# Optimization experiments

Measured on AMD Instinct MI355X. Metric: run time of the kernel, lower is better.

## Reference

```python
import jax, jax.numpy as jnp
import numpy as np

DIM = 1024
CTX_DIM = 768

def setup_inputs() -> dict:
    key = jax.random.key(0)
    ks = jax.random.split(key, 12)
    B, Sq, Skv = 8, 2048, 2048
    s_d = 1.0 / np.sqrt(DIM)
    s_c = 1.0 / np.sqrt(CTX_DIM)
    return {
        "x": jax.random.normal(ks[0], (B, Sq, DIM), jnp.float32),
        "context": jax.random.normal(ks[1], (B, Skv, CTX_DIM), jnp.float32),
        # nn.Linear weights are [out_features, in_features]
        "Wq": jax.random.uniform(ks[2], (DIM, DIM), jnp.float32, -s_d, s_d),
        "bq": jax.random.uniform(ks[3], (DIM,), jnp.float32, -s_d, s_d),
        "Wk": jax.random.uniform(ks[4], (DIM, CTX_DIM), jnp.float32, -s_c, s_c),
        "bk": jax.random.uniform(ks[5], (DIM,), jnp.float32, -s_c, s_c),
        "Wv": jax.random.uniform(ks[6], (DIM, CTX_DIM), jnp.float32, -s_c, s_c),
        "bv": jax.random.uniform(ks[7], (DIM,), jnp.float32, -s_c, s_c),
        "Wo": jax.random.uniform(ks[8], (DIM, DIM), jnp.float32, -s_d, s_d),
        "bo": jax.random.uniform(ks[9], (DIM,), jnp.float32, -s_d, s_d),
    }

def reference(x, context, Wq, bq, Wk, bk, Wv, bv, Wo, bo):
    # q: [B,Sq,D], k,v: [B,Skv,D]
    q = jnp.einsum('bsi,di->bsd', x, Wq) + bq
    k = jnp.einsum('bsc,dc->bsd', context, Wk) + bk
    v = jnp.einsum('bsc,dc->bsd', context, Wv) + bv
    scale = 1.0 / jnp.sqrt(jnp.asarray(q.shape[-1], q.dtype))
    scores = jnp.einsum('bqd,bkd->bqk', q, k) * scale  # [B,Sq,Skv]
    att = jax.nn.softmax(scores, axis=-1)
    out = jnp.einsum('bqk,bkd->bqd', att, v)
    return jnp.einsum('bqd,od->bqo', out, Wo) + bo
```

## Files before the change

### kernel.cpp

```cpp
#include <hip/hip_runtime.h>

typedef unsigned short u16;
typedef unsigned int   u32;
typedef __attribute__((ext_vector_type(8))) short short8;
typedef __attribute__((ext_vector_type(4))) float f32x4;

#define DIM   1024
#define CDIM  768
#define BATCH 8
#define SQ    2048
#define SKV   2048

__device__ __forceinline__ u16 f2bf(float f) {
    union { float f; u32 u; } c; c.f = f;
    u32 u = c.u;
    u += 0x7fffu + ((u >> 16) & 1u);
    return (u16)(u >> 16);
}

__device__ __forceinline__ void async_copy16(const u16* g, u16* l) {
    __builtin_amdgcn_global_load_lds(
        (const __attribute__((address_space(1))) void*)g,
        (__attribute__((address_space(3))) void*)l,
        16, 0, 0);
}

__device__ __forceinline__ void cvt4(const float* s, u16* d, int i) {
    float4 f = ((const float4*)s)[i];
    ushort4 o;
    o.x = f2bf(f.x); o.y = f2bf(f.y); o.z = f2bf(f.z); o.w = f2bf(f.w);
    ((ushort4*)d)[i] = o;
}

__global__ __launch_bounds__(256)
void conv_xc(const float* __restrict__ x, const float* __restrict__ ctx,
             u16* __restrict__ dx, u16* __restrict__ dc)
{
    int i = blockIdx.x * 256 + threadIdx.x;
    if (i < 4194304) cvt4(x, dx, i);
    else             cvt4(ctx, dc, i - 4194304);
}

__global__ __launch_bounds__(256)
void conv_w(const float* __restrict__ Wq, const float* __restrict__ Wk,
            const float* __restrict__ Wv, const float* __restrict__ Wo,
            u16* __restrict__ dq, u16* __restrict__ dk,
            u16* __restrict__ dv, u16* __restrict__ dw)
{
    int i = blockIdx.x * 256 + threadIdx.x;
    if      (i < 262144) cvt4(Wq, dq, i);
    else if (i < 458752) cvt4(Wk, dk, i - 262144);
    else if (i < 655360) cvt4(Wv, dv, i - 458752);
    else                 cvt4(Wo, dw, i - 655360);
}

__device__ __forceinline__ void stage_half(const u16* __restrict__ G, long ld, long k0,
                                           u16* lbase, int h, int w, int lane)
{
    const int srow = lane >> 3;
    const int sch  = (lane & 7) ^ srow;
#pragma unroll
    for (int q = 0; q < 2; ++q) {
        int rb = h * 128 + q * 64 + w * 8;
        async_copy16(G + (long)(rb + srow) * ld + k0 + sch * 8, lbase + rb * 64);
    }
}


#define BARRIER()                                                              \
    do {                                                                       \
        asm volatile("" ::: "memory");                                         \
        __builtin_amdgcn_s_barrier();                                          \
        asm volatile("" ::: "memory");                                         \
    } while (0)

#define LOAD_A(Xs, mh)                                                         \
    do {                                                                       \
        _Pragma("unroll") for (int kc = 0; kc < 2; ++kc)                       \
        _Pragma("unroll") for (int i = 0; i < 4; ++i) {                        \
            int R = wm * 128 + (mh) * 64 + i * 16 + l15;                       \
            a[kc][i] = *(const short8*)&(Xs)[R * 64 +                          \
                         (((kc * 4 + quad) ^ (l15 & 7)) * 8)];                 \
        }                                                                      \
    } while (0)

#define LOAD_B(Xs, nh, dst)                                                    \
    do {                                                                       \
        _Pragma("unroll") for (int kc = 0; kc < 2; ++kc)                       \
        _Pragma("unroll") for (int j = 0; j < 2; ++j) {                        \
            int R = wn * 64 + (nh) * 32 + j * 16 + l15;                        \
            dst[kc][j] = *(const short8*)&(Xs)[R * 64 +                        \
                         (((kc * 4 + quad) ^ (l15 & 7)) * 8)];                 \
        }                                                                      \
    } while (0)

#define MFMA_Q(mh, nh, bb)                                                     \
    do {                                                                       \
        _Pragma("unroll") for (int kc = 0; kc < 2; ++kc)                       \
        _Pragma("unroll") for (int i = 0; i < 4; ++i)                          \
        _Pragma("unroll") for (int j = 0; j < 2; ++j)                          \
            acc[(mh) * 4 + i][(nh) * 2 + j] =                                  \
                __builtin_amdgcn_mfma_f32_16x16x32_bf16(                       \
                    a[kc][i], bb[kc][j],                                       \
                    acc[(mh) * 4 + i][(nh) * 2 + j], 0, 0, 0);                 \
    } while (0)

#define TILE_ITER(CUR, TT)                                                     \
    do {                                                                       \
        u16* As = &smem[CUR][0][0];                                            \
        u16* Bs = &smem[CUR][1][0];                                            \
        u16* An = &smem[(CUR) ^ 1][0][0];                                      \
                                                \
        LOAD_A(As, 0);                                                         \
        LOAD_B(Bs, 0, b0);                                                     \
        if ((TT) + 1 < NT)                                                     \
            stage_half(gA, lda, ((long)(TT) + 1) * 64, An, 0, w, lane);        \
        BARRIER();                                                             \
        asm volatile("s_waitcnt lgkmcnt(0)" ::: "memory");                     \
        __builtin_amdgcn_s_setprio(1);                                         \
        MFMA_Q(0, 0, b0);                                                      \
        __builtin_amdgcn_s_setprio(0);                                         \
        BARRIER();                                                             \
                                                \
        LOAD_B(Bs, 1, b1);                                                     \
        if ((TT) + 1 < NT)                                                     \
            stage_half(gA, lda, ((long)(TT) + 1) * 64, An, 1, w, lane);        \
        BARRIER();                                                             \
        asm volatile("s_waitcnt lgkmcnt(0)" ::: "memory");                     \
        __builtin_amdgcn_s_setprio(1);                                         \
        MFMA_Q(0, 1, b1);                                                      \
        __builtin_amdgcn_s_setprio(0);                                         \
        BARRIER();                                                             \
                                                \
        LOAD_A(As, 1);                                                         \
        if ((TT) + 2 < NT)                                                     \
            stage_half(gB, ldb, ((long)(TT) + 2) * 64, Bs, 0, w, lane);        \
        BARRIER();                                                             \
        asm volatile("s_waitcnt lgkmcnt(0)" ::: "memory");                     \
        __builtin_amdgcn_s_setprio(1);                                         \
        MFMA_Q(1, 0, b0);                                                      \
        __builtin_amdgcn_s_setprio(0);                                         \
        BARRIER();                                                             \
                                                \
        if ((TT) + 2 < NT) {                                                   \
            stage_half(gB, ldb, ((long)(TT) + 2) * 64, Bs, 1, w, lane);        \
            asm volatile("s_waitcnt vmcnt(4)" ::: "memory");                   \
        } else if ((TT) + 1 < NT) {                                            \
            asm volatile("s_waitcnt vmcnt(0)" ::: "memory");                   \
        }                                                                      \
        __builtin_amdgcn_sched_barrier(0);                                     \
        BARRIER();                                                             \
        __builtin_amdgcn_s_setprio(1);                                         \
        MFMA_Q(1, 1, b1);                                                      \
        __builtin_amdgcn_s_setprio(0);                                         \
        BARRIER();                                                             \
    } while (0)

template<int BIAS_MODE, int OUT_MODE>
__global__ __launch_bounds__(512, 2)
void gemm_nt(const u16* __restrict__ A, int lda_, long sA,
             const u16* __restrict__ Bw, int ldb_, long sB,
             const float* __restrict__ bias,
             void* __restrict__ Cout, int ldc_, long sC,
             int K, float scale, float* __restrict__ lsum)
{
    __shared__ u16 smem[2][2][256 * 64];
    const int t    = threadIdx.x;
    const int lane = t & 63;
    const int w    = t >> 6;
    const int wm   = w >> 2;
    const int wn   = w & 3;
    const int l15  = lane & 15;
    const int quad = lane >> 4;
    const long lda = lda_, ldb = ldb_, ldc = ldc_;
    const long m0 = (long)blockIdx.x * 256;
    const long n0 = (long)blockIdx.y * 256;
    const u16* gA = A  + (long)blockIdx.z * sA + m0 * lda;
    const u16* gB = Bw + (long)blockIdx.z * sB + n0 * ldb;
    const int NT = K >> 6;

    short8 a[2][4], b0[2][2], b1[2][2];
    const f32x4 fz = {0.f, 0.f, 0.f, 0.f};
    f32x4 acc[8][4];
#pragma unroll
    for (int i = 0; i < 8; ++i)
#pragma unroll
        for (int j = 0; j < 4; ++j) acc[i][j] = fz;

    stage_half(gA, lda, 0, &smem[0][0][0], 0, w, lane);
    stage_half(gA, lda, 0, &smem[0][0][0], 1, w, lane);
    stage_half(gB, ldb, 0, &smem[0][1][0], 0, w, lane);
    stage_half(gB, ldb, 0, &smem[0][1][0], 1, w, lane);
    if (NT > 1) {
        stage_half(gB, ldb, 64, &smem[1][1][0], 0, w, lane);
        stage_half(gB, ldb, 64, &smem[1][1][0], 1, w, lane);
        asm volatile("s_waitcnt vmcnt(4)" ::: "memory");
    } else {
        asm volatile("s_waitcnt vmcnt(0)" ::: "memory");
    }
    __builtin_amdgcn_sched_barrier(0);
    BARRIER();

    for (int T = 0; T < NT; T += 2) {
        TILE_ITER(0, T);
        TILE_ITER(1, T + 1);
    }

    float invl[8][4];
    if (BIAS_MODE == 3) {
        const long lbase = (long)blockIdx.z * (long)gridDim.x * 256 + m0 + wm * 128;
#pragma unroll
        for (int mi = 0; mi < 8; ++mi)
#pragma unroll
            for (int r = 0; r < 4; ++r)
                invl[mi][r] = 1.f / lsum[lbase + mi * 16 + quad * 4 + r];
    }

    float rowpart[8][4];
    if (OUT_MODE == 2) {
#pragma unroll
        for (int mi = 0; mi < 8; ++mi)
#pragma unroll
            for (int r = 0; r < 4; ++r) rowpart[mi][r] = 0.f;
    }

#pragma unroll
    for (int mi = 0; mi < 8; ++mi) {
#pragma unroll
        for (int nj = 0; nj < 4; ++nj) {
            long n = n0 + wn * 64 + nj * 16 + l15;
#pragma unroll
            for (int r = 0; r < 4; ++r) {
                long m = m0 + wm * 128 + mi * 16 + quad * 4 + r;
                float v = acc[mi][nj][r];
                if (BIAS_MODE == 0) v += bias[n];
                else if (BIAS_MODE == 1) v += bias[m];
                v *= scale;
                if (OUT_MODE == 2) { v = __expf(v); rowpart[mi][r] += v; }
                if (BIAS_MODE == 3) v *= invl[mi][r];
                long off = (long)blockIdx.z * sC + m * ldc + n;
                if (OUT_MODE == 1) ((float*)Cout)[off] = v;
                else               ((u16*)Cout)[off]   = f2bf(v);
            }
        }
    }

    if (OUT_MODE == 2) {
#pragma unroll
        for (int mi = 0; mi < 8; ++mi)
#pragma unroll
            for (int r = 0; r < 4; ++r) {
                float p = rowpart[mi][r];
                p += __shfl_xor(p, 1);
                p += __shfl_xor(p, 2);
                p += __shfl_xor(p, 4);
                p += __shfl_xor(p, 8);
                if (l15 == 0)
                    atomicAdd(&lsum[(long)blockIdx.z * (long)gridDim.x * 256 +
                                    m0 + wm * 128 + mi * 16 + quad * 4 + r], p);
            }
    }
}

extern "C" void kernel_launch(void* const* d_in, const int* in_sizes, int n_in,
                              void* d_out, int out_size, void* d_ws, size_t ws_size,
                              hipStream_t stream)
{
    const float* x   = (const float*)d_in[0];
    const float* ctx = (const float*)d_in[1];
    const float* Wq  = (const float*)d_in[2];
    const float* bq  = (const float*)d_in[3];
    const float* Wk  = (const float*)d_in[4];
    const float* bk  = (const float*)d_in[5];
    const float* Wv  = (const float*)d_in[6];
    const float* bv  = (const float*)d_in[7];
    const float* Wo  = (const float*)d_in[8];
    const float* bo  = (const float*)d_in[9];

    const int MQ  = BATCH * SQ;
    const int NX  = MQ * DIM;
    const int NC  = MQ * CDIM;
    const int NWQ = DIM * DIM;
    const int NWK = DIM * CDIM;

    u16* ws     = (u16*)d_ws;
    u16* xo_bf  = ws;
    u16* ctx_bf = xo_bf + NX;
    u16* k_bf   = ctx_bf + NC;
    u16* vt_bf  = k_bf + NX;
    u16* wq_bf  = vt_bf + NX;
    u16* wk_bf  = wq_bf + NWQ;
    u16* wv_bf  = wk_bf + NWK;
    u16* wo_bf  = wv_bf + NWK;
    u16* S      = wo_bf + NWQ;
    float* lsum = (float*)(S + (long)MQ * SKV);
    u16* q_bf   = (u16*)d_out;

    hipMemsetAsync(lsum, 0, MQ * sizeof(float), stream);

    conv_xc<<<(NX + NC) / 1024, 256, 0, stream>>>(x, ctx, xo_bf, ctx_bf);
    conv_w<<<(2 * NWQ + 2 * NWK) / 1024, 256, 0, stream>>>(
        Wq, Wk, Wv, Wo, wq_bf, wk_bf, wv_bf, wo_bf);

    gemm_nt<0, 0><<<dim3(MQ / 256, DIM / 256, 1), 512, 0, stream>>>(
        xo_bf, DIM, 0, wq_bf, DIM, 0, bq, q_bf, DIM, 0, DIM, 0.03125f, nullptr);
    gemm_nt<0, 0><<<dim3(MQ / 256, DIM / 256, 1), 512, 0, stream>>>(
        ctx_bf, CDIM, 0, wk_bf, CDIM, 0, bk, k_bf, DIM, 0, CDIM, 1.0f, nullptr);
    gemm_nt<1, 0><<<dim3(DIM / 256, MQ / 256, 1), 512, 0, stream>>>(
        wv_bf, CDIM, 0, ctx_bf, CDIM, 0, bv, vt_bf, MQ, 0, CDIM, 1.0f, nullptr);

    gemm_nt<2, 2><<<dim3(SQ / 256, SKV / 256, BATCH), 512, 0, stream>>>(
        q_bf, DIM, (long)SQ * DIM, k_bf, DIM, (long)SKV * DIM,
        nullptr, S, SKV, (long)SQ * SKV, DIM, 1.0f, lsum);

    gemm_nt<3, 0><<<dim3(SQ / 256, DIM / 256, BATCH), 512, 0, stream>>>(
        S, SKV, (long)SQ * SKV, vt_bf, MQ, (long)SKV,
        nullptr, xo_bf, DIM, (long)SQ * DIM, SKV, 1.0f, lsum);

    gemm_nt<0, 1><<<dim3(MQ / 256, DIM / 256, 1), 512, 0, stream>>>(
        xo_bf, DIM, 0, wo_bf, DIM, 0, bo, d_out, DIM, 0, DIM, 1.0f, nullptr);
}
```

Baseline: 459.3 us.

## Rework GEMM staging order and waitcnts for finer-grained LDS pipelining

```diff
diff --git a/kernel.cpp b/kernel.cpp
--- a/kernel.cpp
+++ b/kernel.cpp
@@ -54,25 +54,33 @@
     else                 cvt4(Wo, dw, i - 655360);
 }
 
-__device__ __forceinline__ void stage_half(const u16* __restrict__ G, long ld, long k0,
-                                           u16* lbase, int h, int w, int lane)
+__device__ __forceinline__ void stage_A(const u16* __restrict__ G, long ld, long k0,
+                                        u16* lbase, int p, int w, int lane)
 {
     const int srow = lane >> 3;
     const int sch  = (lane & 7) ^ srow;
 #pragma unroll
     for (int q = 0; q < 2; ++q) {
-        int rb = h * 128 + q * 64 + w * 8;
+        int rb = q * 128 + p * 64 + w * 8;
         async_copy16(G + (long)(rb + srow) * ld + k0 + sch * 8, lbase + rb * 64);
     }
 }
 
-
-#define BARRIER()                                                              \
-    do {                                                                       \
-        asm volatile("" ::: "memory");                                         \
-        __builtin_amdgcn_s_barrier();                                          \
-        asm volatile("" ::: "memory");                                         \
-    } while (0)
+__device__ __forceinline__ void stage_B(const u16* __restrict__ G, long ld, long k0,
+                                        u16* lbase, int p, int w, int lane)
+{
+    const int srow = lane >> 3;
+    const int sch  = (lane & 7) ^ srow;
+#pragma unroll
+    for (int q = 0; q < 2; ++q) {
+        int rb = q * 128 + (w >> 2) * 64 + p * 32 + (w & 3) * 8;
+        async_copy16(G + (long)(rb + srow) * ld + k0 + sch * 8, lbase + rb * 64);
+    }
+}
+
+
+#define SB() __builtin_amdgcn_sched_barrier(0)
+#define FENCE_BAR() do { SB(); __builtin_amdgcn_s_barrier(); SB(); } while (0)
 
 #define LOAD_A(Xs, mh)                                                         \
     do {                                                                       \
@@ -110,50 +118,50 @@
         u16* As = &smem[CUR][0][0];                                            \
         u16* Bs = &smem[CUR][1][0];                                            \
         u16* An = &smem[(CUR) ^ 1][0][0];                                      \
+        const long kA = kcl((TT) + 1);                                         \
+        const long kB = kcl((TT) + 2);                                         \
                                                 \
         LOAD_A(As, 0);                                                         \
         LOAD_B(Bs, 0, b0);                                                     \
-        if ((TT) + 1 < NT)                                                     \
-            stage_half(gA, lda, ((long)(TT) + 1) * 64, An, 0, w, lane);        \
-        BARRIER();                                                             \
-        asm volatile("s_waitcnt lgkmcnt(0)" ::: "memory");                     \
+        stage_A(gA, lda, kA, An, 0, w, lane);                                  \
+        FENCE_BAR();                                                           \
+        asm volatile("s_waitcnt lgkmcnt(0)");                                  \
+        SB();                                                                  \
         __builtin_amdgcn_s_setprio(1);                                         \
         MFMA_Q(0, 0, b0);                                                      \
         __builtin_amdgcn_s_setprio(0);                                         \
-        BARRIER();                                                             \
+        FENCE_BAR();                                                           \
                                                 \
         LOAD_B(Bs, 1, b1);                                                     \
-        if ((TT) + 1 < NT)                                                     \
-            stage_half(gA, lda, ((long)(TT) + 1) * 64, An, 1, w, lane);        \
-        BARRIER();                                                             \
-        asm volatile("s_waitcnt lgkmcnt(0)" ::: "memory");                     \
+        stage_A(gA, lda, kA, An, 1, w, lane);                                  \
+        FENCE_BAR();                                                           \
+        asm volatile("s_waitcnt lgkmcnt(0)");                                  \
+        SB();                                                                  \
         __builtin_amdgcn_s_setprio(1);                                         \
         MFMA_Q(0, 1, b1);                                                      \
         __builtin_amdgcn_s_setprio(0);                                         \
-        BARRIER();                                                             \
+        asm volatile("s_waitcnt vmcnt(8)");                                    \
+        SB();                                                                  \
+        FENCE_BAR();                                                           \
                                                 \
         LOAD_A(As, 1);                                                         \
-        if ((TT) + 2 < NT)                                                     \
-            stage_half(gB, ldb, ((long)(TT) + 2) * 64, Bs, 0, w, lane);        \
-        BARRIER();                                                             \
-        asm volatile("s_waitcnt lgkmcnt(0)" ::: "memory");                     \
+        stage_B(gB, ldb, kB, Bs, 0, w, lane);                                  \
+        FENCE_BAR();                                                           \
+        asm volatile("s_waitcnt lgkmcnt(0)");                                  \
+        SB();                                                                  \
         __builtin_amdgcn_s_setprio(1);                                         \
         MFMA_Q(1, 0, b0);                                                      \
         __builtin_amdgcn_s_setprio(0);                                         \
-        BARRIER();                                                             \
+        FENCE_BAR();                                                           \
                                                 \
-        if ((TT) + 2 < NT) {                                                   \
-            stage_half(gB, ldb, ((long)(TT) + 2) * 64, Bs, 1, w, lane);        \
-            asm volatile("s_waitcnt vmcnt(4)" ::: "memory");                   \
-        } else if ((TT) + 1 < NT) {                                            \
-            asm volatile("s_waitcnt vmcnt(0)" ::: "memory");                   \
-        }                                                                      \
-        __builtin_amdgcn_sched_barrier(0);                                     \
-        BARRIER();                                                             \
+        stage_B(gB, ldb, kB, Bs, 1, w, lane);                                  \
+        FENCE_BAR();                                                           \
         __builtin_amdgcn_s_setprio(1);                                         \
         MFMA_Q(1, 1, b1);                                                      \
         __builtin_amdgcn_s_setprio(0);                                         \
-        BARRIER();                                                             \
+        asm volatile("s_waitcnt vmcnt(6)");                                    \
+        SB();                                                                  \
+        FENCE_BAR();                                                           \
     } while (0)
 
 template<int BIAS_MODE, int OUT_MODE>
@@ -178,6 +186,8 @@
     const u16* gA = A  + (long)blockIdx.z * sA + m0 * lda;
     const u16* gB = Bw + (long)blockIdx.z * sB + n0 * ldb;
     const int NT = K >> 6;
+    const long kmax = (long)K - 64;
+    auto kcl = [&](int tt) -> long { long k = (long)tt * 64; return k < kmax ? k : kmax; };
 
     short8 a[2][4], b0[2][2], b1[2][2];
     const f32x4 fz = {0.f, 0.f, 0.f, 0.f};
@@ -187,19 +197,14 @@
 #pragma unroll
         for (int j = 0; j < 4; ++j) acc[i][j] = fz;
 
-    stage_half(gA, lda, 0, &smem[0][0][0], 0, w, lane);
-    stage_half(gA, lda, 0, &smem[0][0][0], 1, w, lane);
-    stage_half(gB, ldb, 0, &smem[0][1][0], 0, w, lane);
-    stage_half(gB, ldb, 0, &smem[0][1][0], 1, w, lane);
-    if (NT > 1) {
-        stage_half(gB, ldb, 64, &smem[1][1][0], 0, w, lane);
-        stage_half(gB, ldb, 64, &smem[1][1][0], 1, w, lane);
-        asm volatile("s_waitcnt vmcnt(4)" ::: "memory");
-    } else {
-        asm volatile("s_waitcnt vmcnt(0)" ::: "memory");
-    }
-    __builtin_amdgcn_sched_barrier(0);
-    BARRIER();
+    stage_A(gA, lda, 0, &smem[0][0][0], 0, w, lane);
+    stage_A(gA, lda, 0, &smem[0][0][0], 1, w, lane);
+    stage_B(gB, ldb, 0, &smem[0][1][0], 0, w, lane);
+    stage_B(gB, ldb, 0, &smem[0][1][0], 1, w, lane);
+    stage_B(gB, ldb, kcl(1), &smem[1][1][0], 0, w, lane);
+    stage_B(gB, ldb, kcl(1), &smem[1][1][0], 1, w, lane);
+    asm volatile("s_waitcnt vmcnt(4)");
+    FENCE_BAR();
 
     for (int T = 0; T < NT; T += 2) {
         TILE_ITER(0, T);
```

Result: no change. 451.2 us (-1.8%).
